# Optimization experiments

Measured on AMD Instinct MI355X. Metric: run time of the kernel, lower is better.

The kernel has to match this reference:

```python
import jax, jax.numpy as jnp
import numpy as np
from jax import lax

PATCH = 16


def depthwise_conv(x, w):
    # x: (B,C,H,W), w: (C,1,kh,kw) -> SAME padding depthwise conv
    C = x.shape[1]
    return lax.conv_general_dilated(
        x, w, window_strides=(1, 1), padding='SAME',
        feature_group_count=C,
        dimension_numbers=('NCHW', 'OIHW', 'NCHW'))


def get_gradient(x):
    # Sobel-like v/h gradient magnitude per channel (fixed kernels, padding=1)
    C = x.shape[1]
    kv = jnp.array([[0., -1., 0.], [0., 0., 0.], [0., 1., 0.]], dtype=x.dtype)
    kh = jnp.array([[0., 0., 0.], [-1., 0., 1.], [0., 0., 0.]], dtype=x.dtype)
    wv = jnp.broadcast_to(kv[None, None], (C, 1, 3, 3))
    wh = jnp.broadcast_to(kh[None, None], (C, 1, 3, 3))
    gv = depthwise_conv(x, wv)
    gh = depthwise_conv(x, wh)
    return jnp.sqrt(gv * gv + gh * gh + 1e-6)


def patch_resize(x, p=PATCH):
    b, c, h, w = x.shape
    n1, n2 = h // p, w // p
    x = x.reshape(b, c, n1, p, n2, p).transpose(0, 2, 4, 1, 3, 5)
    return x.reshape(b, n1 * n2, c * p * p)


def patch_unresize(x, p=PATCH):
    b, n, l = x.shape
    c = l // (p * p)
    s = int(round(n ** 0.5))
    x = x.reshape(b, s, s, c, p, p).transpose(0, 3, 1, 4, 2, 5)
    return x.reshape(b, c, s * p, s * p)


def setup_inputs() -> dict:
    key = jax.random.key(0)
    k1, k2, k3, k4 = jax.random.split(key, 4)
    hs = jax.random.normal(k1, (4, 128, 512, 512), dtype=jnp.float32)
    ms = jax.random.uniform(k2, (4, 3, 512, 512), dtype=jnp.float32)
    spectral_matrix = jax.random.normal(k3, (128, 3), dtype=jnp.float32) * 0.1
    kernel_weight = jax.random.normal(k4, (3, 1, 3, 3), dtype=jnp.float32) * 0.1
    return {"hs": hs, "ms": ms, "spectral_matrix": spectral_matrix,
            "kernel_weight": kernel_weight}


def reference(hs, ms, spectral_matrix, kernel_weight):
    grad = get_gradient(ms)                               # (B,3,H,W)
    hs_s = jnp.einsum('bchw,cn->bnhw', hs, spectral_matrix)  # (B,3,H,W)
    ms_d = depthwise_conv(ms, kernel_weight)              # learned spatial kernel
    ms_diff = ms - ms_d

    hp = patch_resize(hs_s)                               # (B,N,768)
    mp = patch_resize(ms_d)                               # (B,N,768)
    sim = jnp.einsum('bnd,bmd->bnm', hp, mp)              # (B,N,N)
    soft = jnp.einsum('bnm,bmd->bnd', jax.nn.softmax(sim, axis=-1), mp)
    hard = jnp.argmax(sim, axis=-1)                       # (B,N) int

    hard_matrix = patch_resize(jnp.concatenate([ms, grad, ms_diff], axis=1))  # (B,N,2304)
    gathered = jax.vmap(lambda m, idx: m[idx])(hard_matrix, hard)             # (B,N,2304)

    return jnp.concatenate([patch_unresize(soft), patch_unresize(gathered)], axis=1)
```

## Files before the change

kernel.cpp:

```cpp
#include <hip/hip_runtime.h>

typedef short bf16x8 __attribute__((ext_vector_type(8)));
typedef short bf16x4 __attribute__((ext_vector_type(4)));
typedef float f32x4  __attribute__((ext_vector_type(4)));

__device__ inline unsigned short f2bf(float f){
  unsigned u = __float_as_uint(f);
  u += 0x7fffu + ((u >> 16) & 1u);
  return (unsigned short)(u >> 16);
}
__device__ inline float bf2f(unsigned short s){
  return __uint_as_float(((unsigned)s) << 16);
}
__device__ inline void split3v(float x, short& h, short& m, short& l){
  unsigned short hh = f2bf(x); float r1 = x - bf2f(hh);
  unsigned short mm = f2bf(r1); float r2 = r1 - bf2f(mm);
  h = (short)hh; m = (short)mm; l = (short)f2bf(r2);
}
__device__ inline void split2v(float x, short& h, short& m){
  unsigned short hh = f2bf(x); float r1 = x - bf2f(hh);
  h = (short)hh; m = (short)f2bf(r1);
}

__global__ __launch_bounds__(256) void k_spectral(const float* __restrict__ hs,
                                                  const float* __restrict__ sm,
                                                  short* __restrict__ hph,
                                                  short* __restrict__ hpm,
                                                  short* __restrict__ hpl){
  __shared__ float ssm[384];
  int t = threadIdx.x;
  if (t < 128){ ssm[t] = sm[t]; ssm[t+128] = sm[t+128]; ssm[t+256] = sm[t+256]; }
  __syncthreads();
  int b = blockIdx.y;
  int n = blockIdx.x * 4 + (t >> 6);
  int py  = (t >> 2) & 15;
  int pxq = (t & 3) * 4;
  int y = ((n >> 5) << 4) + py;
  int x = ((n & 31) << 4) + pxq;
  const float* p = hs + (size_t)b * 128 * 262144 + (size_t)y * 512 + x;
  float acc[3][4] = {};
  #pragma unroll 4
  for (int c = 0; c < 128; c++){
    float4 v = *(const float4*)(p + (size_t)c * 262144);
    float w0 = ssm[c*3+0], w1 = ssm[c*3+1], w2 = ssm[c*3+2];
    acc[0][0] = fmaf(v.x, w0, acc[0][0]); acc[0][1] = fmaf(v.y, w0, acc[0][1]);
    acc[0][2] = fmaf(v.z, w0, acc[0][2]); acc[0][3] = fmaf(v.w, w0, acc[0][3]);
    acc[1][0] = fmaf(v.x, w1, acc[1][0]); acc[1][1] = fmaf(v.y, w1, acc[1][1]);
    acc[1][2] = fmaf(v.z, w1, acc[1][2]); acc[1][3] = fmaf(v.w, w1, acc[1][3]);
    acc[2][0] = fmaf(v.x, w2, acc[2][0]); acc[2][1] = fmaf(v.y, w2, acc[2][1]);
    acc[2][2] = fmaf(v.z, w2, acc[2][2]); acc[2][3] = fmaf(v.w, w2, acc[2][3]);
  }
  size_t base = ((size_t)((b << 10) + n)) * 768 + py*16 + pxq;
  #pragma unroll
  for (int c = 0; c < 3; c++){
    short h[4], m[4], l[4];
    #pragma unroll
    for (int e = 0; e < 4; e++) split3v(acc[c][e], h[e], m[e], l[e]);
    *(bf16x4*)(hph + base + c*256) = (bf16x4){h[0],h[1],h[2],h[3]};
    *(bf16x4*)(hpm + base + c*256) = (bf16x4){m[0],m[1],m[2],m[3]};
    *(bf16x4*)(hpl + base + c*256) = (bf16x4){l[0],l[1],l[2],l[3]};
  }
}

__global__ __launch_bounds__(256) void k_msprep(const float* __restrict__ ms,
                                                const float* __restrict__ kw,
                                                short* __restrict__ mph,
                                                short* __restrict__ mpm,
                                                short* __restrict__ mpl){
  int b = blockIdx.y, n = blockIdx.x;
  int Y0 = ((n >> 5) << 4) - 1, X0 = ((n & 31) << 4) - 1;
  __shared__ float win[3][18][18];
  int t = threadIdx.x;
  for (int i = t; i < 972; i += 256){
    int c = i / 324, r = i % 324;
    int yy = Y0 + r / 18, xx = X0 + r % 18;
    win[c][r/18][r%18] = (yy >= 0 && yy < 512 && xx >= 0 && xx < 512)
        ? ms[(size_t)(b*3 + c) * 262144 + (size_t)yy * 512 + xx] : 0.f;
  }
  __syncthreads();
  int py = t >> 4, px = t & 15;
  size_t base = ((size_t)((b << 10) + n)) * 768 + py*16 + px;
  #pragma unroll
  for (int c = 0; c < 3; c++){
    float conv = 0.f;
    #pragma unroll
    for (int dy = 0; dy < 3; dy++)
      #pragma unroll
      for (int dx = 0; dx < 3; dx++)
        conv = fmaf(win[c][py+dy][px+dx], kw[c*9 + dy*3 + dx], conv);
    short h, m, l; split3v(conv, h, m, l);
    mph[base + c*256] = h; mpm[base + c*256] = m; mpl[base + c*256] = l;
  }
}

__global__ __launch_bounds__(256) void k_transpose(const short* __restrict__ src,
                                                   short* __restrict__ dst){
  __shared__ short tile[64][65];
  int n0 = blockIdx.x * 64, d0 = blockIdx.y * 64, b = blockIdx.z;
  const short* s = src + (size_t)b * 786432;
  short* d = dst + (size_t)b * 786432;
  int tx = threadIdx.x & 63, ty = threadIdx.x >> 6;
  #pragma unroll
  for (int i = 0; i < 16; i++){
    int r = i*4 + ty;
    tile[r][tx] = s[(size_t)(n0 + r) * 768 + d0 + tx];
  }
  __syncthreads();
  #pragma unroll
  for (int i = 0; i < 16; i++){
    int r = i*4 + ty;
    d[(size_t)(d0 + r) * 1024 + n0 + tx] = tile[tx][r];
  }
}

template<int MODE, int K, int SA, int SB, int NSPLIT>
__global__ __launch_bounds__(256) void k_gemm(const short* __restrict__ Ah,
                                              const short* __restrict__ Am,
                                              const short* __restrict__ Al,
                                              const short* __restrict__ Bh,
                                              const short* __restrict__ Bm,
                                              const short* __restrict__ Bl,
                                              float* __restrict__ C,
                                              float* __restrict__ out){
  __shared__ short lds[2*NSPLIT][128][40];

  const int t  = threadIdx.x;
  const int b  = blockIdx.z;
  const int n0 = blockIdx.x * 128;
  const int m0 = blockIdx.y * 128;
  const size_t aoff = (size_t)b * 1024 * SA;
  const size_t boff = (size_t)b * (MODE == 0 ? 1024 : 768) * SB;

  const int lane = t & 63;
  const int wid  = t >> 6;
  const int wr = (wid >> 1) * 64;
  const int wc = (wid & 1) * 64;
  const int lrow = lane & 15;
  const int lg   = lane >> 4;

  f32x4 acc[4][4];
  #pragma unroll
  for (int i = 0; i < 4; i++)
    #pragma unroll
    for (int j = 0; j < 4; j++)
      acc[i][j] = (f32x4){0.f, 0.f, 0.f, 0.f};

  for (int k0 = 0; k0 < K; k0 += 32){
    #pragma unroll
    for (int p = 0; p < 2; p++){
      int idx = t + p*256;
      int row = idx >> 2;
      int kc  = (idx & 3) * 8;
      size_t sa = aoff + (size_t)(m0 + row) * SA + k0 + kc;
      size_t sb = boff + (size_t)(n0 + row) * SB + k0 + kc;
      *(bf16x8*)&lds[0][row][kc] = *(const bf16x8*)(Ah + sa);
      *(bf16x8*)&lds[1][row][kc] = *(const bf16x8*)(Am + sa);
      if (NSPLIT == 3) *(bf16x8*)&lds[2][row][kc] = *(const bf16x8*)(Al + sa);
      *(bf16x8*)&lds[NSPLIT+0][row][kc] = *(const bf16x8*)(Bh + sb);
      *(bf16x8*)&lds[NSPLIT+1][row][kc] = *(const bf16x8*)(Bm + sb);
      if (NSPLIT == 3) *(bf16x8*)&lds[NSPLIT+2][row][kc] = *(const bf16x8*)(Bl + sb);
    }
    __syncthreads();

    bf16x8 afh[4], afm[4], afl[4];
    #pragma unroll
    for (int i = 0; i < 4; i++){
      int r = wr + i*16 + lrow;
      afh[i] = *(const bf16x8*)&lds[0][r][lg*8];
      afm[i] = *(const bf16x8*)&lds[1][r][lg*8];
      if (NSPLIT == 3) afl[i] = *(const bf16x8*)&lds[2][r][lg*8];
    }
    #pragma unroll
    for (int j = 0; j < 4; j++){
      int r = wc + j*16 + lrow;
      bf16x8 bh = *(const bf16x8*)&lds[NSPLIT+0][r][lg*8];
      bf16x8 bm = *(const bf16x8*)&lds[NSPLIT+1][r][lg*8];
      bf16x8 bl;
      if (NSPLIT == 3) bl = *(const bf16x8*)&lds[NSPLIT+2][r][lg*8];
      #pragma unroll
      for (int i = 0; i < 4; i++){
        f32x4 c = acc[i][j];
        c = __builtin_amdgcn_mfma_f32_16x16x32_bf16(afh[i], bh, c, 0, 0, 0);
        c = __builtin_amdgcn_mfma_f32_16x16x32_bf16(afh[i], bm, c, 0, 0, 0);
        c = __builtin_amdgcn_mfma_f32_16x16x32_bf16(afm[i], bh, c, 0, 0, 0);
        if (NSPLIT == 3){
          c = __builtin_amdgcn_mfma_f32_16x16x32_bf16(afh[i], bl, c, 0, 0, 0);
          c = __builtin_amdgcn_mfma_f32_16x16x32_bf16(afl[i], bh, c, 0, 0, 0);
          c = __builtin_amdgcn_mfma_f32_16x16x32_bf16(afm[i], bm, c, 0, 0, 0);
        }
        acc[i][j] = c;
      }
    }
    __syncthreads();
  }

  #pragma unroll
  for (int i = 0; i < 4; i++){
    #pragma unroll
    for (int j = 0; j < 4; j++){
      #pragma unroll
      for (int r = 0; r < 4; r++){
        int row = m0 + wr + i*16 + lg*4 + r;
        int col = n0 + wc + j*16 + lrow;
        float val = acc[i][j][r];
        if (MODE == 0){
          C[((size_t)b << 20) + ((size_t)row << 10) + col] = val;
        } else {
          int ch = col >> 8;
          int py = (col >> 4) & 15;
          int px = col & 15;
          int yy = ((row >> 5) << 4) + py;
          int xx = ((row & 31) << 4) + px;
          out[((size_t)(b*12 + ch) * 512 + yy) * 512 + xx] = val;
        }
      }
    }
  }
}

__global__ __launch_bounds__(256) void k_softmax(float* __restrict__ sim,
                                                 int* __restrict__ hard){
  const int row = blockIdx.x;
  float* p = sim + (size_t)row * 1024;
  const int t = threadIdx.x;
  float4 v = ((const float4*)p)[t];

  float mx = v.x; int mi = 0;
  if (v.y > mx){ mx = v.y; mi = 1; }
  if (v.z > mx){ mx = v.z; mi = 2; }
  if (v.w > mx){ mx = v.w; mi = 3; }
  mi += t * 4;
  #pragma unroll
  for (int off = 32; off > 0; off >>= 1){
    float omx = __shfl_down(mx, off);
    int   omi = __shfl_down(mi, off);
    if (omx > mx || (omx == mx && omi < mi)){ mx = omx; mi = omi; }
  }
  __shared__ float wmx[4];
  __shared__ int   wmi[4];
  if ((t & 63) == 0){ wmx[t >> 6] = mx; wmi[t >> 6] = mi; }
  __syncthreads();
  mx = wmx[0]; mi = wmi[0];
  #pragma unroll
  for (int w = 1; w < 4; w++){
    if (wmx[w] > mx || (wmx[w] == mx && wmi[w] < mi)){ mx = wmx[w]; mi = wmi[w]; }
  }

  float e0 = expf(v.x - mx), e1 = expf(v.y - mx);
  float e2 = expf(v.z - mx), e3 = expf(v.w - mx);
  float s = e0 + e1 + e2 + e3;
  #pragma unroll
  for (int off = 32; off > 0; off >>= 1) s += __shfl_down(s, off);
  __shared__ float ws[4];
  if ((t & 63) == 0) ws[t >> 6] = s;
  __syncthreads();
  s = ws[0] + ws[1] + ws[2] + ws[3];
  float inv = 1.f / s;
  float o[4] = {e0*inv, e1*inv, e2*inv, e3*inv};

  __syncthreads();
  short h[4], m[4];
  #pragma unroll
  for (int e = 0; e < 4; e++) split2v(o[e], h[e], m[e]);
  short* rowp = (short*)p;
  *(bf16x4*)(rowp + t*4)        = (bf16x4){h[0],h[1],h[2],h[3]};
  *(bf16x4*)(rowp + 1024 + t*4) = (bf16x4){m[0],m[1],m[2],m[3]};
  if (t == 0) hard[row] = mi;
}

__global__ __launch_bounds__(256) void k_gather(const float* __restrict__ ms,
                                                const float* __restrict__ kw,
                                                const int* __restrict__ hard,
                                                float* __restrict__ out){
  int x = blockIdx.x * 256 + threadIdx.x;
  int y = blockIdx.y;
  int z = blockIdx.z;
  int b = z / 3, c = z % 3;
  int n = ((y >> 4) << 5) + (x >> 4);
  int idx = hard[(b << 10) + n];
  int sy = ((idx >> 5) << 4) + (y & 15);
  int sx = ((idx & 31) << 4) + (x & 15);
  const float* base = ms + (size_t)(b*3 + c) * 262144;
  float v[3][3];
  #pragma unroll
  for (int dy = 0; dy < 3; dy++){
    int yy = sy + dy - 1;
    #pragma unroll
    for (int dx = 0; dx < 3; dx++){
      int xx = sx + dx - 1;
      v[dy][dx] = (yy >= 0 && yy < 512 && xx >= 0 && xx < 512)
                  ? base[(size_t)yy * 512 + xx] : 0.f;
    }
  }
  float conv = 0.f;
  #pragma unroll
  for (int dy = 0; dy < 3; dy++)
    #pragma unroll
    for (int dx = 0; dx < 3; dx++)
      conv = fmaf(v[dy][dx], kw[c*9 + dy*3 + dx], conv);
  float gv = v[2][1] - v[0][1];
  float gh = v[1][2] - v[1][0];
  float g  = sqrtf(gv*gv + gh*gh + 1e-6f);
  float ctr  = v[1][1];
  float diff = ctr - conv;
  size_t o = ((size_t)(b*12 + 3 + c) * 512 + y) * 512 + x;
  out[o]            = ctr;
  out[o + 3*262144] = g;
  out[o + 6*262144] = diff;
}

extern "C" void kernel_launch(void* const* d_in, const int* in_sizes, int n_in,
                              void* d_out, int out_size, void* d_ws, size_t ws_size,
                              hipStream_t stream){
  const float* hs = (const float*)d_in[0];
  const float* ms = (const float*)d_in[1];
  const float* sm = (const float*)d_in[2];
  const float* kw = (const float*)d_in[3];
  float* out = (float*)d_out;

  const size_t CE = 3145728;
  short* w = (short*)d_ws;
  short* hph = w;            short* hpm = hph + CE;  short* hpl = hpm + CE;
  short* mph = hpl + CE;     short* mpm = mph + CE;  short* mpl = mpm + CE;
  short* mpTh = mpl + CE;    short* mpTm = mpTh + CE;
  float* sim = (float*)(mpTm + CE);
  int*   hard = (int*)(sim + 4194304);

  k_spectral <<<dim3(256, 4),    256, 0, stream>>>(hs, sm, hph, hpm, hpl);
  k_msprep   <<<dim3(1024, 4),   256, 0, stream>>>(ms, kw, mph, mpm, mpl);
  k_transpose<<<dim3(16, 12, 4), 256, 0, stream>>>(mph, mpTh);
  k_transpose<<<dim3(16, 12, 4), 256, 0, stream>>>(mpm, mpTm);
  k_gemm<0, 768, 768, 768, 3><<<dim3(8, 8, 4), 256, 0, stream>>>(
      hph, hpm, hpl, mph, mpm, mpl, sim, nullptr);
  k_softmax  <<<dim3(4096),      256, 0, stream>>>(sim, hard);
  k_gemm<1, 1024, 2048, 1024, 2><<<dim3(6, 8, 4), 256, 0, stream>>>(
      (const short*)sim, (const short*)sim + 1024, nullptr,
      mpTh, mpTm, nullptr, nullptr, out);
  k_gather   <<<dim3(2, 512, 12), 256, 0, stream>>>(ms, kw, hard, out);
}
```

Baseline: 868.4 us.

## Coalesce spectral reads, merge transposes, and load GEMM fragments directly from global

The spectral projection kernel now maps threads to consecutive row pixels so each channel read is fully coalesced, and scatters results into patch layout afterwards. The two transpose launches are merged into one grid covering both components. The GEMM drops its LDS staging and barriers, using 512-thread blocks whose 8 waves each load their MFMA fragments straight from global memory. This saves LDS traffic and synchronization, but each fragment is now fetched from global or L2 by several waves, giving more redundant, less coalesced loads.

```diff
diff --git a/kernel.cpp b/kernel.cpp
--- a/kernel.cpp
+++ b/kernel.cpp
@@ -32,30 +32,31 @@
   if (t < 128){ ssm[t] = sm[t]; ssm[t+128] = sm[t+128]; ssm[t+256] = sm[t+256]; }
   __syncthreads();
   int b = blockIdx.y;
-  int n = blockIdx.x * 4 + (t >> 6);
-  int py  = (t >> 2) & 15;
-  int pxq = (t & 3) * 4;
-  int y = ((n >> 5) << 4) + py;
-  int x = ((n & 31) << 4) + pxq;
+  int lin = (blockIdx.x * 256 + t) * 4;
+  int y = lin >> 9;
+  int x = lin & 511;
   const float* p = hs + (size_t)b * 128 * 262144 + (size_t)y * 512 + x;
-  float acc[3][4] = {};
-  #pragma unroll 4
+  float a0[4] = {0,0,0,0}, a1[4] = {0,0,0,0}, a2[4] = {0,0,0,0};
+  #pragma unroll 8
   for (int c = 0; c < 128; c++){
     float4 v = *(const float4*)(p + (size_t)c * 262144);
     float w0 = ssm[c*3+0], w1 = ssm[c*3+1], w2 = ssm[c*3+2];
-    acc[0][0] = fmaf(v.x, w0, acc[0][0]); acc[0][1] = fmaf(v.y, w0, acc[0][1]);
-    acc[0][2] = fmaf(v.z, w0, acc[0][2]); acc[0][3] = fmaf(v.w, w0, acc[0][3]);
-    acc[1][0] = fmaf(v.x, w1, acc[1][0]); acc[1][1] = fmaf(v.y, w1, acc[1][1]);
-    acc[1][2] = fmaf(v.z, w1, acc[1][2]); acc[1][3] = fmaf(v.w, w1, acc[1][3]);
-    acc[2][0] = fmaf(v.x, w2, acc[2][0]); acc[2][1] = fmaf(v.y, w2, acc[2][1]);
-    acc[2][2] = fmaf(v.z, w2, acc[2][2]); acc[2][3] = fmaf(v.w, w2, acc[2][3]);
-  }
-  size_t base = ((size_t)((b << 10) + n)) * 768 + py*16 + pxq;
+    a0[0] = fmaf(v.x, w0, a0[0]); a0[1] = fmaf(v.y, w0, a0[1]);
+    a0[2] = fmaf(v.z, w0, a0[2]); a0[3] = fmaf(v.w, w0, a0[3]);
+    a1[0] = fmaf(v.x, w1, a1[0]); a1[1] = fmaf(v.y, w1, a1[1]);
+    a1[2] = fmaf(v.z, w1, a1[2]); a1[3] = fmaf(v.w, w1, a1[3]);
+    a2[0] = fmaf(v.x, w2, a2[0]); a2[1] = fmaf(v.y, w2, a2[1]);
+    a2[2] = fmaf(v.z, w2, a2[2]); a2[3] = fmaf(v.w, w2, a2[3]);
+  }
+  int n  = ((y >> 4) << 5) + (x >> 4);
+  int db = ((y & 15) << 4) + (x & 15);
+  size_t base = ((size_t)((b << 10) + n)) * 768 + db;
+  float* accs[3] = {a0, a1, a2};
   #pragma unroll
   for (int c = 0; c < 3; c++){
     short h[4], m[4], l[4];
     #pragma unroll
-    for (int e = 0; e < 4; e++) split3v(acc[c][e], h[e], m[e], l[e]);
+    for (int e = 0; e < 4; e++) split3v(accs[c][e], h[e], m[e], l[e]);
     *(bf16x4*)(hph + base + c*256) = (bf16x4){h[0],h[1],h[2],h[3]};
     *(bf16x4*)(hpm + base + c*256) = (bf16x4){m[0],m[1],m[2],m[3]};
     *(bf16x4*)(hpl + base + c*256) = (bf16x4){l[0],l[1],l[2],l[3]};
@@ -93,12 +94,15 @@
   }
 }
 
-__global__ __launch_bounds__(256) void k_transpose(const short* __restrict__ src,
-                                                   short* __restrict__ dst){
+__global__ __launch_bounds__(256) void k_transpose(const short* __restrict__ mph,
+                                                   const short* __restrict__ mpm,
+                                                   short* __restrict__ mpTh,
+                                                   short* __restrict__ mpTm){
   __shared__ short tile[64][65];
-  int n0 = blockIdx.x * 64, d0 = blockIdx.y * 64, b = blockIdx.z;
-  const short* s = src + (size_t)b * 786432;
-  short* d = dst + (size_t)b * 786432;
+  int n0 = blockIdx.x * 64, d0 = blockIdx.y * 64;
+  int b = blockIdx.z >> 1, comp = blockIdx.z & 1;
+  const short* s = (comp ? mpm : mph) + (size_t)b * 786432;
+  short* d = (comp ? mpTm : mpTh) + (size_t)b * 786432;
   int tx = threadIdx.x & 63, ty = threadIdx.x >> 6;
   #pragma unroll
   for (int i = 0; i < 16; i++){
@@ -114,7 +118,7 @@
 }
 
 template<int MODE, int K, int SA, int SB, int NSPLIT>
-__global__ __launch_bounds__(256) void k_gemm(const short* __restrict__ Ah,
+__global__ __launch_bounds__(512) void k_gemm(const short* __restrict__ Ah,
                                               const short* __restrict__ Am,
                                               const short* __restrict__ Al,
                                               const short* __restrict__ Bh,
@@ -122,61 +126,44 @@
                                               const short* __restrict__ Bl,
                                               float* __restrict__ C,
                                               float* __restrict__ out){
-  __shared__ short lds[2*NSPLIT][128][40];
-
   const int t  = threadIdx.x;
   const int b  = blockIdx.z;
   const int n0 = blockIdx.x * 128;
   const int m0 = blockIdx.y * 128;
-  const size_t aoff = (size_t)b * 1024 * SA;
-  const size_t boff = (size_t)b * (MODE == 0 ? 1024 : 768) * SB;
-
   const int lane = t & 63;
   const int wid  = t >> 6;
-  const int wr = (wid >> 1) * 64;
-  const int wc = (wid & 1) * 64;
+  const int wr = (wid >> 2) * 64;
+  const int wc = (wid & 3) * 32;
   const int lrow = lane & 15;
   const int lg   = lane >> 4;
 
-  f32x4 acc[4][4];
+  const size_t abase = (size_t)b * 1024 * SA + (size_t)(m0 + wr + lrow) * SA + lg*8;
+  const size_t bbase = (size_t)b * (size_t)(MODE == 0 ? 1024 : 768) * SB
+                     + (size_t)(n0 + wc + lrow) * SB + lg*8;
+
+  f32x4 acc[4][2];
   #pragma unroll
   for (int i = 0; i < 4; i++)
     #pragma unroll
-    for (int j = 0; j < 4; j++)
+    for (int j = 0; j < 2; j++)
       acc[i][j] = (f32x4){0.f, 0.f, 0.f, 0.f};
 
   for (int k0 = 0; k0 < K; k0 += 32){
-    #pragma unroll
-    for (int p = 0; p < 2; p++){
-      int idx = t + p*256;
-      int row = idx >> 2;
-      int kc  = (idx & 3) * 8;
-      size_t sa = aoff + (size_t)(m0 + row) * SA + k0 + kc;
-      size_t sb = boff + (size_t)(n0 + row) * SB + k0 + kc;
-      *(bf16x8*)&lds[0][row][kc] = *(const bf16x8*)(Ah + sa);
-      *(bf16x8*)&lds[1][row][kc] = *(const bf16x8*)(Am + sa);
-      if (NSPLIT == 3) *(bf16x8*)&lds[2][row][kc] = *(const bf16x8*)(Al + sa);
-      *(bf16x8*)&lds[NSPLIT+0][row][kc] = *(const bf16x8*)(Bh + sb);
-      *(bf16x8*)&lds[NSPLIT+1][row][kc] = *(const bf16x8*)(Bm + sb);
-      if (NSPLIT == 3) *(bf16x8*)&lds[NSPLIT+2][row][kc] = *(const bf16x8*)(Bl + sb);
+    bf16x8 afh[4], afm[4], afl[4];
+    #pragma unroll
+    for (int i = 0; i < 4; i++){
+      size_t sa = abase + (size_t)(i*16) * SA + k0;
+      afh[i] = *(const bf16x8*)(Ah + sa);
+      afm[i] = *(const bf16x8*)(Am + sa);
+      if (NSPLIT == 3) afl[i] = *(const bf16x8*)(Al + sa);
     }
-    __syncthreads();
-
-    bf16x8 afh[4], afm[4], afl[4];
-    #pragma unroll
-    for (int i = 0; i < 4; i++){
-      int r = wr + i*16 + lrow;
-      afh[i] = *(const bf16x8*)&lds[0][r][lg*8];
-      afm[i] = *(const bf16x8*)&lds[1][r][lg*8];
-      if (NSPLIT == 3) afl[i] = *(const bf16x8*)&lds[2][r][lg*8];
-    }
-    #pragma unroll
-    for (int j = 0; j < 4; j++){
-      int r = wc + j*16 + lrow;
-      bf16x8 bh = *(const bf16x8*)&lds[NSPLIT+0][r][lg*8];
-      bf16x8 bm = *(const bf16x8*)&lds[NSPLIT+1][r][lg*8];
+    #pragma unroll
+    for (int j = 0; j < 2; j++){
+      size_t sb = bbase + (size_t)(j*16) * SB + k0;
+      bf16x8 bh = *(const bf16x8*)(Bh + sb);
+      bf16x8 bm = *(const bf16x8*)(Bm + sb);
       bf16x8 bl;
-      if (NSPLIT == 3) bl = *(const bf16x8*)&lds[NSPLIT+2][r][lg*8];
+      if (NSPLIT == 3) bl = *(const bf16x8*)(Bl + sb);
       #pragma unroll
       for (int i = 0; i < 4; i++){
         f32x4 c = acc[i][j];
@@ -191,13 +178,12 @@
         acc[i][j] = c;
       }
     }
-    __syncthreads();
   }
 
   #pragma unroll
   for (int i = 0; i < 4; i++){
     #pragma unroll
-    for (int j = 0; j < 4; j++){
+    for (int j = 0; j < 2; j++){
       #pragma unroll
       for (int r = 0; r < 4; r++){
         int row = m0 + wr + i*16 + lg*4 + r;
@@ -328,12 +314,11 @@
 
   k_spectral <<<dim3(256, 4),    256, 0, stream>>>(hs, sm, hph, hpm, hpl);
   k_msprep   <<<dim3(1024, 4),   256, 0, stream>>>(ms, kw, mph, mpm, mpl);
-  k_transpose<<<dim3(16, 12, 4), 256, 0, stream>>>(mph, mpTh);
-  k_transpose<<<dim3(16, 12, 4), 256, 0, stream>>>(mpm, mpTm);
-  k_gemm<0, 768, 768, 768, 3><<<dim3(8, 8, 4), 256, 0, stream>>>(
+  k_transpose<<<dim3(16, 12, 8), 256, 0, stream>>>(mph, mpm, mpTh, mpTm);
+  k_gemm<0, 768, 768, 768, 3><<<dim3(8, 8, 4), 512, 0, stream>>>(
       hph, hpm, hpl, mph, mpm, mpl, sim, nullptr);
   k_softmax  <<<dim3(4096),      256, 0, stream>>>(sim, hard);
-  k_gemm<1, 1024, 2048, 1024, 2><<<dim3(6, 8, 4), 256, 0, stream>>>(
+  k_gemm<1, 1024, 2048, 1024, 2><<<dim3(6, 8, 4), 512, 0, stream>>>(
       (const short*)sim, (const short*)sim + 1024, nullptr,
       mpTh, mpTm, nullptr, nullptr, out);
   k_gather   <<<dim3(2, 512, 12), 256, 0, stream>>>(ms, kw, hard, out);
```

Measured after the change: 938.5 us. 8.1% more time.
